# Kernel optimization log

Measured on AMD Instinct MI355X. Metric: run time of the kernel, lower is better.

The kernel has to match this reference:

```python
import jax, jax.numpy as jnp
import numpy as np

TAU = 0.5
EPS = 1e-12


def _projection(z, W1, b1, W2, b2):
    # fc2(elu(fc1(z)))
    h = jax.nn.elu(z @ W1 + b1)
    return h @ W2 + b2


def _l2_normalize(z):
    n = jnp.linalg.norm(z, axis=1, keepdims=True)
    return z / jnp.maximum(n, EPS)


def _semi_loss(h1, h2, tau):
    n1 = _l2_normalize(h1)
    n2 = _l2_normalize(h2)
    refl = jnp.exp((n1 @ n1.T) / tau)      # [N, N]
    between = jnp.exp((n1 @ n2.T) / tau)   # [N, N]
    denom = refl.sum(axis=1) + between.sum(axis=1) - jnp.diagonal(refl)
    return -jnp.log(jnp.diagonal(between) / denom)


def setup_inputs() -> dict:
    key = jax.random.key(0)
    k1, k2, k3, k4 = jax.random.split(key, 4)
    N, H, P = 12288, 256, 256
    s = 1.0 / np.sqrt(H)
    return {
        "z1": jax.random.normal(k1, (N, H), dtype=jnp.float32),
        "z2": jax.random.normal(k2, (N, H), dtype=jnp.float32),
        "W1": jax.random.normal(k3, (H, P), dtype=jnp.float32) * s,
        "b1": jnp.zeros((P,), dtype=jnp.float32),
        "W2": jax.random.normal(k4, (P, H), dtype=jnp.float32) * s,
        "b2": jnp.zeros((H,), dtype=jnp.float32),
    }


def reference(z1, z2, W1, b1, W2, b2):
    h1 = _projection(z1, W1, b1, W2, b2)
    h2 = _projection(z2, W1, b1, W2, b2)
    l1 = _semi_loss(h1, h2, TAU)
    l2 = _semi_loss(h2, h1, TAU)
    return ((l1 + l2) * 0.5).mean()
```

## Files before the change

### kernel.cpp

```cpp
#include <hip/hip_runtime.h>
#include <hip/hip_bf16.h>

typedef __attribute__((ext_vector_type(4))) float f32x4;
typedef __attribute__((ext_vector_type(8))) short bf16x8;

#define NR 12288
#define HD 256
#define TAU 0.5f
#define NU 24576
#define NTT 192
#define NSUB 384
#define NBLK (NTT * (NTT + 1) / 2)

__device__ __forceinline__ unsigned short f2bf(float f) {
    unsigned int x = __builtin_bit_cast(unsigned int, f);
    x += 0x7fffu + ((x >> 16) & 1u);
    return (unsigned short)(x >> 16);
}

__device__ __forceinline__ unsigned char f2e4m3(float f) {
    unsigned int u = __builtin_bit_cast(unsigned int, f);
    unsigned int s = (u >> 24) & 0x80u;
    float af = fabsf(f);
    if (af >= 464.f) return (unsigned char)(s | 0x7Eu);
    if (af < 0.015625f) {
        unsigned int q = (unsigned int)(af * 512.f + 0.5f);
        return (unsigned char)(s | q);
    }
    int e = (int)((u >> 23) & 0xffu) - 127;
    unsigned int mant = u & 0x7fffffu;
    unsigned int val = (unsigned int)((e + 7) << 3) | (mant >> 20);
    unsigned int rem = mant & 0xfffffu;
    val += (rem > 0x80000u) || (rem == 0x80000u && (val & 1u));
    return (unsigned char)(s | val);
}

__global__ __launch_bounds__(256) void cast4_kernel(const float* __restrict__ src,
                                                    unsigned short* __restrict__ dst, int n4) {
    int i = blockIdx.x * 256 + threadIdx.x;
    if (i >= n4) return;
    float4 v = ((const float4*)src)[i];
    ushort4 u;
    u.x = f2bf(v.x); u.y = f2bf(v.y); u.z = f2bf(v.z); u.w = f2bf(v.w);
    ((ushort4*)dst)[i] = u;
}

__global__ __launch_bounds__(256) void transpose_cast_kernel(const float* __restrict__ W,
                                                             unsigned short* __restrict__ Wt) {
    int n = blockIdx.x;
    int k = threadIdx.x;
    Wt[n * HD + k] = f2bf(W[k * HD + n]);
}

template <int ELU>
__global__ __launch_bounds__(256) void proj_kernel(const unsigned short* __restrict__ A,
                                                   const unsigned short* __restrict__ Bt,
                                                   const float* __restrict__ bias,
                                                   void* __restrict__ Cout) {
    const int lane = threadIdx.x & 63;
    const int wave = threadIdx.x >> 6;
    const int row0 = blockIdx.x * 64;
    const int col0 = wave * 64;
    const int lr = lane & 15, lk = lane >> 4;

    f32x4 acc[4][4] = {};
    const unsigned short* Ab = A + (size_t)(row0 + lr) * HD + lk * 8;
    const unsigned short* Bb = Bt + (size_t)(col0 + lr) * HD + lk * 8;
#pragma unroll
    for (int k0 = 0; k0 < HD; k0 += 32) {
        bf16x8 af[4], bfr[4];
#pragma unroll
        for (int m = 0; m < 4; ++m) af[m] = *(const bf16x8*)(Ab + m * 16 * HD + k0);
#pragma unroll
        for (int n = 0; n < 4; ++n) bfr[n] = *(const bf16x8*)(Bb + n * 16 * HD + k0);
#pragma unroll
        for (int m = 0; m < 4; ++m)
#pragma unroll
            for (int n = 0; n < 4; ++n)
                acc[m][n] = __builtin_amdgcn_mfma_f32_16x16x32_bf16(af[m], bfr[n], acc[m][n], 0, 0, 0);
    }
#pragma unroll
    for (int m = 0; m < 4; ++m) {
#pragma unroll
        for (int n = 0; n < 4; ++n) {
            int col = col0 + n * 16 + lr;
            float b = bias[col];
#pragma unroll
            for (int r = 0; r < 4; ++r) {
                int row = row0 + m * 16 + lk * 4 + r;
                float v = acc[m][n][r] + b;
                if (ELU) {
                    v = v > 0.f ? v : expm1f(v);
                    ((unsigned short*)Cout)[(size_t)row * HD + col] = f2bf(v);
                } else {
                    ((float*)Cout)[(size_t)row * HD + col] = v;
                }
            }
        }
    }
}

__global__ __launch_bounds__(256) void norm_diag_kernel(const float* __restrict__ h1,
                                                        const float* __restrict__ h2,
                                                        unsigned char* __restrict__ n1,
                                                        unsigned char* __restrict__ n2,
                                                        float* __restrict__ dvec) {
    const int lane = threadIdx.x & 63;
    const int wave = threadIdx.x >> 6;
    const int row = blockIdx.x * 4 + wave;
    const float4 a = *(const float4*)(h1 + (size_t)row * HD + lane * 4);
    const float4 b = *(const float4*)(h2 + (size_t)row * HD + lane * 4);
    float sa = a.x * a.x + a.y * a.y + a.z * a.z + a.w * a.w;
    float sb = b.x * b.x + b.y * b.y + b.z * b.z + b.w * b.w;
    float sab = a.x * b.x + a.y * b.y + a.z * b.z + a.w * b.w;
#pragma unroll
    for (int m = 32; m; m >>= 1) {
        sa += __shfl_xor(sa, m);
        sb += __shfl_xor(sb, m);
        sab += __shfl_xor(sab, m);
    }
    float na = sqrtf(sa); na = na > 1e-12f ? na : 1e-12f;
    float nb = sqrtf(sb); nb = nb > 1e-12f ? nb : 1e-12f;
    float ia = 1.f / na, ib = 1.f / nb;
    uchar4 q1, q2;
    q1.x = f2e4m3(a.x * ia); q1.y = f2e4m3(a.y * ia); q1.z = f2e4m3(a.z * ia); q1.w = f2e4m3(a.w * ia);
    q2.x = f2e4m3(b.x * ib); q2.y = f2e4m3(b.y * ib); q2.z = f2e4m3(b.z * ib); q2.w = f2e4m3(b.w * ib);
    const int sw = ((row >> 3) & 1) << 3;
    *(uchar4*)(n1 + (size_t)row * HD + ((lane * 4) ^ sw)) = q1;
    *(uchar4*)(n2 + (size_t)row * HD + ((lane * 4) ^ sw)) = q2;
    if (lane == 0) dvec[row] = sab * ia * ib * (1.f / TAU);
}

__global__ __launch_bounds__(256, 2) void gram_kernel(const unsigned char* __restrict__ nU8,
                                                      float* __restrict__ RPART) {
    __shared__ __align__(16) unsigned char lA[128 * 256];
    __shared__ __align__(16) unsigned char lB[128 * 256];

    const int bid = blockIdx.x;
    const int t0 = (bid & 7) * (NBLK / 8) + (bid >> 3);
    int i = (int)((385.f - sqrtf((float)(385 * 385 - 8 * t0))) * 0.5f);
    if (i < 0) i = 0;
    if (i > NTT - 1) i = NTT - 1;
    while (i > 0 && i * NTT - i * (i - 1) / 2 > t0) --i;
    while ((i + 1) * NTT - (i + 1) * i / 2 <= t0) ++i;
    const int j = i + (t0 - (i * NTT - i * (i - 1) / 2));
    const bool diag = (i == j);

    const unsigned char* X = nU8 + (size_t)i * 128 * HD;
    const unsigned char* Y = nU8 + (size_t)j * 128 * HD;

    const int t = threadIdx.x;
    const int lane = t & 63;
    const int wave = t >> 6;
    const int wr = wave >> 1, wc = wave & 1;
    const int lr = lane & 15, lk = lane >> 4;

    {
        const int rbase = t >> 4;
        const int schunk = (t & 15) ^ rbase;
        const unsigned char* gx = X + rbase * 256 + schunk * 16;
        const unsigned char* gy = Y + rbase * 256 + schunk * 16;
#pragma unroll
        for (int c = 0; c < 8; ++c) {
            __builtin_amdgcn_global_load_lds(
                (const __attribute__((address_space(1))) unsigned int*)(gx + c * 4096),
                (__attribute__((address_space(3))) unsigned int*)(&lA[c * 4096 + t * 16]),
                16, 0, 0);
        }
        if (!diag) {
#pragma unroll
            for (int c = 0; c < 8; ++c) {
                __builtin_amdgcn_global_load_lds(
                    (const __attribute__((address_space(1))) unsigned int*)(gy + c * 4096),
                    (__attribute__((address_space(3))) unsigned int*)(&lB[c * 4096 + t * 16]),
                    16, 0, 0);
            }
        }
    }
    __syncthreads();

    f32x4 acc[4][4] = {};
    const int hswap = (lr >> 3) & 1;
    const unsigned char* sA = lA + (size_t)(wr * 64 + lr) * 256 + ((lk & 1) ^ hswap) * 8;
    const unsigned char* sBb = (diag ? lA : lB);
    const unsigned char* sB = sBb + (size_t)(wc * 64 + lr) * 256 + ((lk & 1) ^ hswap) * 8;
#pragma unroll
    for (int ks = 0; ks < 8; ++ks) {
        const int chnk = ((2 * ks + (lk >> 1)) ^ lr) * 16;
        long af[4], bfr[4];
#pragma unroll
        for (int m = 0; m < 4; ++m)
            af[m] = *(const long*)(sA + m * 16 * 256 + chnk);
#pragma unroll
        for (int n = 0; n < 4; ++n)
            bfr[n] = *(const long*)(sB + n * 16 * 256 + chnk);
#pragma unroll
        for (int m = 0; m < 4; ++m)
#pragma unroll
            for (int n = 0; n < 4; ++n)
                acc[m][n] = __builtin_amdgcn_mfma_f32_16x16x32_fp8_fp8(af[m], bfr[n], acc[m][n], 0, 0, 0);
    }

    const float kexp = 2.8853901f;
#pragma unroll
    for (int m = 0; m < 4; ++m)
#pragma unroll
        for (int n = 0; n < 4; ++n)
#pragma unroll
            for (int r = 0; r < 4; ++r)
                acc[m][n][r] = exp2f(acc[m][n][r] * kexp);

    {
        float* dst = RPART + (size_t)(2 * j + wc) * NU + i * 128 + wr * 64;
#pragma unroll
        for (int m = 0; m < 4; ++m) {
            float rs[4];
#pragma unroll
            for (int r = 0; r < 4; ++r) {
                rs[r] = acc[m][0][r] + acc[m][1][r] + acc[m][2][r] + acc[m][3][r];
                rs[r] += __shfl_xor(rs[r], 1);
                rs[r] += __shfl_xor(rs[r], 2);
                rs[r] += __shfl_xor(rs[r], 4);
                rs[r] += __shfl_xor(rs[r], 8);
            }
            if (lr == 0) {
#pragma unroll
                for (int r = 0; r < 4; ++r) dst[m * 16 + lk * 4 + r] = rs[r];
            }
        }
    }
    if (!diag) {
        float* dst = RPART + (size_t)(2 * i + wr) * NU + j * 128 + wc * 64;
#pragma unroll
        for (int n = 0; n < 4; ++n) {
            float cs = 0.f;
#pragma unroll
            for (int m = 0; m < 4; ++m)
#pragma unroll
                for (int r = 0; r < 4; ++r) cs += acc[m][n][r];
            cs += __shfl_xor(cs, 16);
            cs += __shfl_xor(cs, 32);
            if (lk == 0) dst[n * 16 + lr] = cs;
        }
    }
}

__global__ __launch_bounds__(256) void reduce_part_kernel(const float* __restrict__ RPART,
                                                          float* __restrict__ S) {
    const int r = blockIdx.x * 256 + threadIdx.x;
    float s = 0.f;
#pragma unroll 8
    for (int p = 0; p < NSUB; ++p) s += RPART[(size_t)p * NU + r];
    S[r] = s;
}

__global__ __launch_bounds__(128) void loss_partial_kernel(const float* __restrict__ S,
                                                           const float* __restrict__ dvec,
                                                           float* __restrict__ partial) {
    int i = blockIdx.x * 128 + threadIdx.x;
    const float e2 = 7.389056099f;
    float d = dvec[i];
    float l1 = logf(S[i] - e2) - d;
    float l2 = logf(S[NR + i] - e2) - d;
    float v = 0.5f * (l1 + l2);
#pragma unroll
    for (int m = 32; m; m >>= 1) v += __shfl_xor(v, m);
    __shared__ float wsum[2];
    if ((threadIdx.x & 63) == 0) wsum[threadIdx.x >> 6] = v;
    __syncthreads();
    if (threadIdx.x == 0) partial[blockIdx.x] = wsum[0] + wsum[1];
}

__global__ __launch_bounds__(128) void loss_final_kernel(const float* __restrict__ partial,
                                                         float* __restrict__ out, int nb) {
    float s = 0.f;
    for (int i = threadIdx.x; i < nb; i += 128) s += partial[i];
#pragma unroll
    for (int m = 32; m; m >>= 1) s += __shfl_xor(s, m);
    __shared__ float wsum[2];
    if ((threadIdx.x & 63) == 0) wsum[threadIdx.x >> 6] = s;
    __syncthreads();
    if (threadIdx.x == 0) out[0] = (wsum[0] + wsum[1]) * (1.f / (float)NR);
}

extern "C" void kernel_launch(void* const* d_in, const int* in_sizes, int n_in,
                              void* d_out, int out_size, void* d_ws, size_t ws_size,
                              hipStream_t stream) {
    const float* z1 = (const float*)d_in[0];
    const float* z2 = (const float*)d_in[1];
    const float* W1 = (const float*)d_in[2];
    const float* b1 = (const float*)d_in[3];
    const float* W2 = (const float*)d_in[4];
    const float* b2 = (const float*)d_in[5];

    char* ws = (char*)d_ws;
    size_t off = 0;
    auto alloc = [&](size_t bytes) {
        void* p = ws + off;
        off += (bytes + 255) & ~(size_t)255;
        return p;
    };
    const size_t NH2 = (size_t)NR * HD * 2;
    unsigned short* zb1 = (unsigned short*)alloc(NH2);
    unsigned short* zb2 = (unsigned short*)alloc(NH2);
    unsigned short* W1t = (unsigned short*)alloc(HD * HD * 2);
    unsigned short* W2t = (unsigned short*)alloc(HD * HD * 2);
    unsigned short* t1 = (unsigned short*)alloc(NH2);
    unsigned short* t2 = (unsigned short*)alloc(NH2);
    float* h1 = (float*)alloc((size_t)NR * HD * 4);
    float* h2 = (float*)alloc((size_t)NR * HD * 4);
    unsigned char* nU = (unsigned char*)alloc((size_t)NU * HD);
    float* S = (float*)alloc((size_t)NU * 4);
    float* dvec = (float*)alloc(NR * 4);
    float* partial = (float*)alloc(96 * 4);
    float* RPART = (float*)ws;

    const int n4 = NR * HD / 4;
    cast4_kernel<<<(n4 + 255) / 256, 256, 0, stream>>>(z1, zb1, n4);
    cast4_kernel<<<(n4 + 255) / 256, 256, 0, stream>>>(z2, zb2, n4);
    transpose_cast_kernel<<<HD, 256, 0, stream>>>(W1, W1t);
    transpose_cast_kernel<<<HD, 256, 0, stream>>>(W2, W2t);

    proj_kernel<1><<<NR / 64, 256, 0, stream>>>(zb1, W1t, b1, t1);
    proj_kernel<1><<<NR / 64, 256, 0, stream>>>(zb2, W1t, b1, t2);
    proj_kernel<0><<<NR / 64, 256, 0, stream>>>(t1, W2t, b2, h1);
    proj_kernel<0><<<NR / 64, 256, 0, stream>>>(t2, W2t, b2, h2);

    norm_diag_kernel<<<NR / 4, 256, 0, stream>>>(h1, h2, nU, nU + (size_t)NR * HD, dvec);

    hipMemsetAsync(RPART, 0, (size_t)NSUB * NU * 4, stream);

    gram_kernel<<<NBLK, 256, 0, stream>>>(nU, RPART);

    reduce_part_kernel<<<NU / 256, 256, 0, stream>>>(RPART, S);

    loss_partial_kernel<<<NR / 128, 128, 0, stream>>>(S, dvec, partial);
    loss_final_kernel<<<1, 128, 0, stream>>>(partial, (float*)d_out, NR / 128);
}
```

Baseline: 312.2 us.

## Split gram tiles across eight waves and store bf16 row-sum partials

The gram kernel now runs 512 threads per block, with each wave computing a 64x32 sub-tile instead of 64x64. This roughly halves the accumulators per wave and doubles the waves available to hide LDS and MFMA latency. Row-sum partials are stored as bf16 and the partition count doubles to 768, so the partial buffer stays the same size in bytes. The bf16 rounding of partial sums adds precision risk to the final log-sum.

Measured after the change: 340.6 us. 1.09x slower.

```diff
diff --git a/kernel.cpp b/kernel.cpp
--- a/kernel.cpp
+++ b/kernel.cpp
@@ -9,13 +9,18 @@
 #define TAU 0.5f
 #define NU 24576
 #define NTT 192
-#define NSUB 384
+#define NSUB 768
 #define NBLK (NTT * (NTT + 1) / 2)
 
 __device__ __forceinline__ unsigned short f2bf(float f) {
     unsigned int x = __builtin_bit_cast(unsigned int, f);
     x += 0x7fffu + ((x >> 16) & 1u);
     return (unsigned short)(x >> 16);
+}
+
+__device__ __forceinline__ float bf2f(unsigned short b) {
+    unsigned int u = ((unsigned int)b) << 16;
+    return __builtin_bit_cast(float, u);
 }
 
 __device__ __forceinline__ unsigned char f2e4m3(float f) {
@@ -131,8 +136,8 @@
     if (lane == 0) dvec[row] = sab * ia * ib * (1.f / TAU);
 }
 
-__global__ __launch_bounds__(256, 2) void gram_kernel(const unsigned char* __restrict__ nU8,
-                                                      float* __restrict__ RPART) {
+__global__ __launch_bounds__(512, 2) void gram_kernel(const unsigned char* __restrict__ nU8,
+                                                      unsigned short* __restrict__ RPART) {
     __shared__ __align__(16) unsigned char lA[128 * 256];
     __shared__ __align__(16) unsigned char lB[128 * 256];
 
@@ -152,52 +157,52 @@
     const int t = threadIdx.x;
     const int lane = t & 63;
     const int wave = t >> 6;
-    const int wr = wave >> 1, wc = wave & 1;
+    const int wr = wave >> 2, wc = wave & 3;
     const int lr = lane & 15, lk = lane >> 4;
 
     {
-        const int rbase = t >> 4;
-        const int schunk = (t & 15) ^ rbase;
-        const unsigned char* gx = X + rbase * 256 + schunk * 16;
-        const unsigned char* gy = Y + rbase * 256 + schunk * 16;
-#pragma unroll
-        for (int c = 0; c < 8; ++c) {
+        const int srow = t >> 4;
+        const int schunk = (t & 15) ^ (srow & 15);
+        const unsigned char* gx = X + srow * 256 + schunk * 16;
+        const unsigned char* gy = Y + srow * 256 + schunk * 16;
+#pragma unroll
+        for (int c = 0; c < 4; ++c) {
             __builtin_amdgcn_global_load_lds(
-                (const __attribute__((address_space(1))) unsigned int*)(gx + c * 4096),
-                (__attribute__((address_space(3))) unsigned int*)(&lA[c * 4096 + t * 16]),
+                (const __attribute__((address_space(1))) unsigned int*)(gx + c * 8192),
+                (__attribute__((address_space(3))) unsigned int*)(&lA[c * 8192 + t * 16]),
                 16, 0, 0);
         }
         if (!diag) {
 #pragma unroll
-            for (int c = 0; c < 8; ++c) {
+            for (int c = 0; c < 4; ++c) {
                 __builtin_amdgcn_global_load_lds(
-                    (const __attribute__((address_space(1))) unsigned int*)(gy + c * 4096),
-                    (__attribute__((address_space(3))) unsigned int*)(&lB[c * 4096 + t * 16]),
+                    (const __attribute__((address_space(1))) unsigned int*)(gy + c * 8192),
+                    (__attribute__((address_space(3))) unsigned int*)(&lB[c * 8192 + t * 16]),
                     16, 0, 0);
             }
         }
     }
     __syncthreads();
 
-    f32x4 acc[4][4] = {};
+    f32x4 acc[4][2] = {};
     const int hswap = (lr >> 3) & 1;
     const unsigned char* sA = lA + (size_t)(wr * 64 + lr) * 256 + ((lk & 1) ^ hswap) * 8;
     const unsigned char* sBb = (diag ? lA : lB);
-    const unsigned char* sB = sBb + (size_t)(wc * 64 + lr) * 256 + ((lk & 1) ^ hswap) * 8;
+    const unsigned char* sB = sBb + (size_t)(wc * 32 + lr) * 256 + ((lk & 1) ^ hswap) * 8;
 #pragma unroll
     for (int ks = 0; ks < 8; ++ks) {
         const int chnk = ((2 * ks + (lk >> 1)) ^ lr) * 16;
-        long af[4], bfr[4];
+        long af[4], bfr[2];
 #pragma unroll
         for (int m = 0; m < 4; ++m)
             af[m] = *(const long*)(sA + m * 16 * 256 + chnk);
 #pragma unroll
-        for (int n = 0; n < 4; ++n)
+        for (int n = 0; n < 2; ++n)
             bfr[n] = *(const long*)(sB + n * 16 * 256 + chnk);
 #pragma unroll
         for (int m = 0; m < 4; ++m)
 #pragma unroll
-            for (int n = 0; n < 4; ++n)
+            for (int n = 0; n < 2; ++n)
                 acc[m][n] = __builtin_amdgcn_mfma_f32_16x16x32_fp8_fp8(af[m], bfr[n], acc[m][n], 0, 0, 0);
     }
 
@@ -205,19 +210,19 @@
 #pragma unroll
     for (int m = 0; m < 4; ++m)
 #pragma unroll
-        for (int n = 0; n < 4; ++n)
+        for (int n = 0; n < 2; ++n)
 #pragma unroll
             for (int r = 0; r < 4; ++r)
                 acc[m][n][r] = exp2f(acc[m][n][r] * kexp);
 
     {
-        float* dst = RPART + (size_t)(2 * j + wc) * NU + i * 128 + wr * 64;
+        unsigned short* dst = RPART + (size_t)(4 * j + wc) * NU + i * 128 + wr * 64;
 #pragma unroll
         for (int m = 0; m < 4; ++m) {
             float rs[4];
 #pragma unroll
             for (int r = 0; r < 4; ++r) {
-                rs[r] = acc[m][0][r] + acc[m][1][r] + acc[m][2][r] + acc[m][3][r];
+                rs[r] = acc[m][0][r] + acc[m][1][r];
                 rs[r] += __shfl_xor(rs[r], 1);
                 rs[r] += __shfl_xor(rs[r], 2);
                 rs[r] += __shfl_xor(rs[r], 4);
@@ -225,14 +230,14 @@
             }
             if (lr == 0) {
 #pragma unroll
-                for (int r = 0; r < 4; ++r) dst[m * 16 + lk * 4 + r] = rs[r];
+                for (int r = 0; r < 4; ++r) dst[m * 16 + lk * 4 + r] = f2bf(rs[r]);
             }
         }
     }
     if (!diag) {
-        float* dst = RPART + (size_t)(2 * i + wr) * NU + j * 128 + wc * 64;
-#pragma unroll
-        for (int n = 0; n < 4; ++n) {
+        unsigned short* dst = RPART + (size_t)(2 * i + wr) * NU + j * 128 + wc * 32;
+#pragma unroll
+        for (int n = 0; n < 2; ++n) {
             float cs = 0.f;
 #pragma unroll
             for (int m = 0; m < 4; ++m)
@@ -240,17 +245,17 @@
                 for (int r = 0; r < 4; ++r) cs += acc[m][n][r];
             cs += __shfl_xor(cs, 16);
             cs += __shfl_xor(cs, 32);
-            if (lk == 0) dst[n * 16 + lr] = cs;
-        }
-    }
-}
-
-__global__ __launch_bounds__(256) void reduce_part_kernel(const float* __restrict__ RPART,
+            if (lk == 0) dst[n * 16 + lr] = f2bf(cs);
+        }
+    }
+}
+
+__global__ __launch_bounds__(256) void reduce_part_kernel(const unsigned short* __restrict__ RPART,
                                                           float* __restrict__ S) {
     const int r = blockIdx.x * 256 + threadIdx.x;
     float s = 0.f;
 #pragma unroll 8
-    for (int p = 0; p < NSUB; ++p) s += RPART[(size_t)p * NU + r];
+    for (int p = 0; p < NSUB; ++p) s += bf2f(RPART[(size_t)p * NU + r]);
     S[r] = s;
 }
 
@@ -313,7 +318,7 @@
     float* S = (float*)alloc((size_t)NU * 4);
     float* dvec = (float*)alloc(NR * 4);
     float* partial = (float*)alloc(96 * 4);
-    float* RPART = (float*)ws;
+    unsigned short* RPART = (unsigned short*)ws;
 
     const int n4 = NR * HD / 4;
     cast4_kernel<<<(n4 + 255) / 256, 256, 0, stream>>>(z1, zb1, n4);
@@ -328,9 +333,9 @@
 
     norm_diag_kernel<<<NR / 4, 256, 0, stream>>>(h1, h2, nU, nU + (size_t)NR * HD, dvec);
 
-    hipMemsetAsync(RPART, 0, (size_t)NSUB * NU * 4, stream);
-
-    gram_kernel<<<NBLK, 256, 0, stream>>>(nU, RPART);
+    hipMemsetAsync(RPART, 0, (size_t)NSUB * NU * 2, stream);
+
+    gram_kernel<<<NBLK, 512, 0, stream>>>(nU, RPART);
 
     reduce_part_kernel<<<NU / 256, 256, 0, stream>>>(RPART, S);
 
```
